# Performance work log

Hardware: AMD Instinct MI355X
Metric: run time of the kernel (lower is better)

Reference implementation:

```python
import jax, jax.numpy as jnp
import numpy as np

# Config constants (match init_kwargs)
E = 16          # n_routed_experts
G = 4           # n_groups
TOPK_G = 2      # topk_groups
K = 4           # n_activated_experts
ROUTE_SCALE = 2.5446


def setup_inputs() -> dict:
    key = jax.random.key(0)
    ks = jax.random.split(key, 9)
    T, D, H = 2048, 1024, 704
    HS = 2 * H  # shared FFN hidden = n_shared_experts * expert_hidden_dim
    sc = lambda k, shape, fan_in: (jax.random.normal(k, shape, jnp.float32)
                                   * (fan_in ** -0.5))
    return {
        "x":      jax.random.normal(ks[0], (T, D), jnp.float32),
        "gate_w": sc(ks[1], (E, D), D),
        "gate_b": jnp.zeros((E,), jnp.float32),       # V3 routing bias (init 0)
        "w1":     sc(ks[2], (E, H, D), D),            # gate proj per expert
        "w3":     sc(ks[3], (E, H, D), D),            # up proj per expert
        "w2":     sc(ks[4], (E, D, H), H),            # down proj per expert
        "ws1":    sc(ks[5], (HS, D), D),              # shared FFN gate proj
        "ws3":    sc(ks[6], (HS, D), D),              # shared FFN up proj
        "ws2":    sc(ks[7], (D, HS), HS),             # shared FFN down proj
    }


def _gate(x, gate_w, gate_b):
    """DeepSeek-V3 sigmoid gate with bias routing + group-limited masking."""
    T = x.shape[0]
    logits = x @ gate_w.T                                   # [T, E]
    scores = jax.nn.sigmoid(logits).astype(jnp.float32)     # original_scores
    routing = scores + gate_b                               # bias only affects routing
    g = routing.reshape(T, G, E // G)
    # use_bias=True -> group score = sum of top-2 routing scores in group
    group_scores = jnp.sum(jax.lax.top_k(g, 2)[0], axis=-1)     # [T, G]
    top_groups = jax.lax.top_k(group_scores, TOPK_G)[1]         # [T, TOPK_G]
    keep = jnp.any(jnp.arange(G)[None, :, None] == top_groups[:, None, :],
                   axis=-1)                                     # [T, G]
    routing = jnp.where(keep[:, :, None], g, -jnp.inf).reshape(T, E)
    idx = jax.lax.top_k(routing, K)[1]                          # [T, K]
    w = jnp.take_along_axis(scores, idx, axis=1)                # un-biased weights
    w = w / jnp.clip(jnp.sum(w, axis=-1, keepdims=True), 1e-9)  # sigmoid renorm
    w = (w * ROUTE_SCALE).astype(x.dtype)
    return w, idx


def reference(x, gate_w, gate_b, w1, w3, w2, ws1, ws3, ws2):
    T, D = x.shape
    weights, idx = _gate(x, gate_w, gate_b)                 # [T,K], [T,K]
    # Dense dispatch/combine matrix: combine[t, e] = gate weight (0 if unrouted)
    combine = jnp.zeros((T, E), x.dtype).at[
        jnp.arange(T)[:, None], idx].add(weights)           # [T, E]
    # Routed experts: SwiGLU per expert, grouped GEMMs
    hg = jnp.einsum('td,ehd->eth', x, w1)                   # [E, T, H]
    hu = jnp.einsum('td,ehd->eth', x, w3)                   # [E, T, H]
    eo = jnp.einsum('eth,edh->etd', jax.nn.silu(hg) * hu, w2)  # [E, T, D]
    y_routed = jnp.einsum('etd,te->td', eo, combine)        # [T, D]
    # Shared experts (always active SwiGLU)
    y_shared = (jax.nn.silu(x @ ws1.T) * (x @ ws3.T)) @ ws2.T
    return y_routed + y_shared
```

## Files before the change

kernel.cpp:

```cpp
#include <hip/hip_runtime.h>
#include <hip/hip_bf16.h>
#include <math.h>

typedef __attribute__((ext_vector_type(4))) float   f32x4;
typedef __attribute__((ext_vector_type(8))) short   short8;
typedef __attribute__((ext_vector_type(8))) __bf16  bf16x8;

union SB8 { short8 s; bf16x8 b; };

__device__ __forceinline__ short f2bf(float f) {
  union { float f; unsigned u; } v; v.f = f;
  unsigned r = v.u + 0x7fffu + ((v.u >> 16) & 1u);
  return (short)(r >> 16);
}

__device__ __forceinline__ short8 cvt8(f32x4 a, f32x4 b) {
  short8 r;
  r[0] = f2bf(a[0]); r[1] = f2bf(a[1]); r[2] = f2bf(a[2]); r[3] = f2bf(a[3]);
  r[4] = f2bf(b[0]); r[5] = f2bf(b[1]); r[6] = f2bf(b[2]); r[7] = f2bf(b[3]);
  return r;
}

__device__ __forceinline__ void ldsload16(const short* g, short* l) {
  __builtin_amdgcn_global_load_lds(
      (const __attribute__((address_space(1))) unsigned int*)g,
      (__attribute__((address_space(3))) unsigned int*)l, 16, 0, 0);
}

#define TT   2048
#define DD   1024
#define HH   704
#define HSS  1408
#define EE   16
#define CAP  2048
#define CSTR 32

#define O1  2097152ULL
#define O2  13631488ULL
#define O3  25165824ULL
#define O4  36700160ULL
#define O5  38141952ULL
#define O6  39583744ULL
#define CVT_TOTAL 41025536ULL

#define W2SZ    11534336ULL
#define WS1SZ   1441792ULL
#define WS1END  26607616ULL
#define CVTA_TOTAL  28049408ULL
#define CVTA_BLOCKS 3424
#define GATE_BLOCKS 512

__global__ __launch_bounds__(256)
void gate_cvt(const float* __restrict__ x,  const float* __restrict__ w1,
              const float* __restrict__ w3, const float* __restrict__ s1,
              const float* __restrict__ s3, short* __restrict__ dst,
              const float* __restrict__ gw, const float* __restrict__ gb,
              int* __restrict__ counts, int* __restrict__ tok,
              float* __restrict__ wgt, int* __restrict__ eslot)
{
  if (blockIdx.x >= GATE_BLOCKS) {
    const int tid = threadIdx.x;
    const size_t base = (size_t)(blockIdx.x - GATE_BLOCKS) * 8192;
    const float* sp[4]; short* dp[4];
    #pragma unroll
    for (int k = 0; k < 4; k++) {
      const size_t sb = base + (size_t)k * 2048;
      const float* src; size_t doff;
      if      (sb < O1)     { src = x  + sb;            doff = sb; }
      else if (sb < O2)     { src = w1 + (sb - O1);     doff = sb; }
      else if (sb < O3)     { src = w3 + (sb - O2);     doff = sb; }
      else if (sb < WS1END) { src = s1 + (sb - O3);     doff = sb + W2SZ; }
      else                  { src = s3 + (sb - WS1END); doff = sb + W2SZ; }
      sp[k] = src + tid * 8;
      dp[k] = dst + doff + tid * 8;
    }
    f32x4 va[8];
    #pragma unroll
    for (int k = 0; k < 4; k++) {
      va[2 * k]     = *(const f32x4*)(sp[k]);
      va[2 * k + 1] = *(const f32x4*)(sp[k] + 4);
    }
    #pragma unroll
    for (int k = 0; k < 4; k++)
      *(short8*)(dp[k]) = cvt8(va[2 * k], va[2 * k + 1]);
    return;
  }

  const int lane = threadIdx.x & 63;
  const int wid  = threadIdx.x >> 6;
  const int t    = blockIdx.x * 4 + wid;
  const int e    = lane & 15;
  const int p    = lane >> 4;

  const float* xp = x + (size_t)t * DD + p * 256;
  const float* gp = gw + (size_t)e * DD + p * 256;

  double a0 = 0.0, a1 = 0.0, a2 = 0.0, a3 = 0.0;
  #pragma unroll 8
  for (int i = 0; i < 64; i++) {
    f32x4 xa = *(const f32x4*)(xp + i * 4);
    f32x4 ga = *(const f32x4*)(gp + i * 4);
    a0 += (double)xa[0] * (double)ga[0];
    a1 += (double)xa[1] * (double)ga[1];
    a2 += (double)xa[2] * (double)ga[2];
    a3 += (double)xa[3] * (double)ga[3];
  }
  double acc = (a0 + a1) + (a2 + a3);
  acc += __shfl_xor(acc, 16);
  acc += __shfl_xor(acc, 32);
  float accf = (float)acc;

  float lf[EE], sc[EE], r[EE];
  #pragma unroll
  for (int j = 0; j < EE; j++) lf[j] = __shfl(accf, j);
  #pragma unroll
  for (int j = 0; j < EE; j++) {
    sc[j] = 1.f / (1.f + expf(-lf[j]));
    r[j] = sc[j] + gb[j];
  }
  float gs[4];
  #pragma unroll
  for (int g = 0; g < 4; g++) {
    float m1 = -1e30f, m2 = -1e30f;
    #pragma unroll
    for (int j = 0; j < 4; j++) {
      float v = r[g * 4 + j];
      if (v > m1) { m2 = m1; m1 = v; }
      else if (v > m2) { m2 = v; }
    }
    gs[g] = m1 + m2;
  }
  int g1 = 0, g2 = -1; float b1 = -1e30f, b2 = -1e30f;
  #pragma unroll
  for (int g = 0; g < 4; g++) {
    if (gs[g] > b1) { b2 = b1; g2 = g1; b1 = gs[g]; g1 = g; }
    else if (gs[g] > b2) { b2 = gs[g]; g2 = g; }
  }
  int idx[4]; float wv[4]; float wsum = 0.f;
  unsigned used = 0;
  #pragma unroll
  for (int k = 0; k < 4; k++) {
    float best = -1e30f; int bi = 0;
    #pragma unroll
    for (int j = 0; j < EE; j++) {
      int g = j >> 2;
      bool keep = (g == g1) || (g == g2);
      if (keep && !((used >> j) & 1) && r[j] > best) { best = r[j]; bi = j; }
    }
    used |= 1u << bi; idx[k] = bi; wv[k] = sc[bi]; wsum += sc[bi];
  }
  float div = wsum < 1e-9f ? 1e-9f : wsum;
  if (lane < 4) {
    float w = wv[lane] / div * 2.5446f;
    int slot = atomicAdd(&counts[idx[lane] * CSTR], 1);
    tok[idx[lane] * CAP + slot] = t;
    wgt[idx[lane] * CAP + slot] = w;
    eslot[t * 4 + lane] = (idx[lane] << 16) | slot;
  }
}

#define WAIT_PREV_TILE()  do { \
    asm volatile("s_waitcnt vmcnt(8)" ::: "memory"); \
    __builtin_amdgcn_sched_barrier(0); \
    __builtin_amdgcn_s_barrier(); \
    __builtin_amdgcn_sched_barrier(0); } while (0)
#define WAIT_LAST_TILE()  do { \
    asm volatile("s_waitcnt vmcnt(0)" ::: "memory"); \
    __builtin_amdgcn_sched_barrier(0); \
    __builtin_amdgcn_s_barrier(); \
    __builtin_amdgcn_sched_barrier(0); } while (0)
#define END_TILE_BARRIER() do { \
    __builtin_amdgcn_sched_barrier(0); \
    __builtin_amdgcn_s_barrier(); } while (0)

__global__ __launch_bounds__(256, 2)
void gemm1_merged(const short* __restrict__ xb, const short* __restrict__ w1b,
                  const short* __restrict__ w3b, const short* __restrict__ ws1b,
                  const short* __restrict__ ws3b, short* __restrict__ act_r,
                  short* __restrict__ act_s, const int* __restrict__ counts,
                  const int* __restrict__ tok,
                  const float* __restrict__ w2f, const float* __restrict__ ws2f,
                  short* __restrict__ w2bd, short* __restrict__ ws2bd)
{
  const int F = blockIdx.x + 11 * (blockIdx.y + 16 * blockIdx.z);
  const int r8 = F & 7, rank = F >> 3;
  int z, Mt, Ntc;
  if (rank < 22) {
    z = 0;
    const int p = rank * 8 + r8;
    Mt = p / 11; Ntc = p - Mt * 11;
  } else if (rank < 374) {
    const int rr = rank - 22;
    z = 1 + r8 + 8 * (rr / 176);
    const int p = rr % 176;
    Mt = p / 11; Ntc = p - Mt * 11;
  } else {
    z = 17;
    const int p = (rank - 374) * 8 + r8;
    Mt = p / 22; Ntc = p - Mt * 22;
  }

  if (z == 0) {
    const int bid = Mt * 11 + Ntc;
    const int tid = threadIdx.x;
    for (int s = 0; s < 9; s++) {
      const size_t base = (size_t)bid * 73728 + (size_t)s * 8192;
      const float* sp[4]; short* dp[4];
      #pragma unroll
      for (int k = 0; k < 4; k++) {
        const size_t sb = base + (size_t)k * 2048;
        if (sb < W2SZ) {
          sp[k] = w2f + sb + tid * 8;
          dp[k] = w2bd + sb + tid * 8;
        } else {
          const size_t o = sb - W2SZ;
          sp[k] = ws2f + o + tid * 8;
          dp[k] = ws2bd + o + tid * 8;
        }
      }
      f32x4 va[8];
      #pragma unroll
      for (int k = 0; k < 4; k++) {
        va[2 * k]     = *(const f32x4*)(sp[k]);
        va[2 * k + 1] = *(const f32x4*)(sp[k] + 4);
      }
      #pragma unroll
      for (int k = 0; k < 4; k++)
        *(short8*)(dp[k]) = cvt8(va[2 * k], va[2 * k + 1]);
    }
    return;
  }

  const bool routed = (z <= EE);
  const int e = z - 1;

  int cnt, N, rowbase = 0;
  const short *W1, *W3;
  short* act;
  if (routed) {
    cnt = counts[e * CSTR];
    if (Mt * 128 >= cnt) return;
    int rb = 0;
    for (int i = 0; i < e; i++) rb += counts[i * CSTR];
    rowbase = rb;
    N = HH;
    W1 = w1b + (size_t)e * HH * DD;
    W3 = w3b + (size_t)e * HH * DD;
    act = act_r;
  } else {
    cnt = TT; N = HSS; W1 = ws1b; W3 = ws3b; act = act_s;
  }
  const int NtB = Ntc * 64;

  __shared__ __align__(16) short lA [2][128 * 64];
  __shared__ __align__(16) short lB1[2][64 * 64];
  __shared__ __align__(16) short lB3[2][64 * 64];

  const int tid = threadIdx.x, lane = tid & 63, wv = tid >> 6;
  const int srow = lane >> 3, schunk = lane & 7, scg = schunk ^ srow;

  const short* pa[4]; const short* pb1[2]; const short* pb3[2];
  #pragma unroll
  for (int i = 0; i < 4; i++) {
    const int g = wv * 4 + i;
    int arow = Mt * 128 + g * 8 + srow;
    if (routed) {
      int slot = arow < cnt ? arow : cnt - 1;
      arow = tok[e * CAP + slot];
    }
    pa[i] = xb + (size_t)arow * DD + scg * 8;
  }
  #pragma unroll
  for (int i = 0; i < 2; i++) {
    const int g = wv * 2 + i;
    const int brow = NtB + g * 8 + srow;
    pb1[i] = W1 + (size_t)brow * DD + scg * 8;
    pb3[i] = W3 + (size_t)brow * DD + scg * 8;
  }

  f32x4 acc1[8], acc3[8];
  #pragma unroll
  for (int i = 0; i < 8; i++) { acc1[i] = (f32x4)0.f; acc3[i] = (f32x4)0.f; }

  const int q = lane >> 4, r7 = lane & 7, hi = (lane & 15) >> 3;

#define STAGE1(c, kk) do { \
    _Pragma("unroll") for (int i = 0; i < 4; i++) \
      ldsload16(pa[i] + (kk),  &lA [c][(wv * 4 + i) * 512]); \
    _Pragma("unroll") for (int i = 0; i < 2; i++) { \
      ldsload16(pb1[i] + (kk), &lB1[c][(wv * 2 + i) * 512]); \
      ldsload16(pb3[i] + (kk), &lB3[c][(wv * 2 + i) * 512]); } } while (0)

#define GEMM1_BODY(c) do { \
    _Pragma("unroll") for (int kc = 0; kc < 2; kc++) { \
      const int cx = (kc * 4 + q) ^ r7; \
      SB8 b1f, b3f; \
      b1f.s = *(const short8*)(&lB1[c][((wv * 2 + hi) * 64 + r7 * 8 + cx) * 8]); \
      b3f.s = *(const short8*)(&lB3[c][((wv * 2 + hi) * 64 + r7 * 8 + cx) * 8]); \
      _Pragma("unroll") for (int mt = 0; mt < 8; mt++) { \
        SB8 af; af.s = *(const short8*)(&lA[c][((2 * mt + hi) * 64 + r7 * 8 + cx) * 8]); \
        acc1[mt] = __builtin_amdgcn_mfma_f32_16x16x32_bf16(af.b, b1f.b, acc1[mt], 0, 0, 0); \
        acc3[mt] = __builtin_amdgcn_mfma_f32_16x16x32_bf16(af.b, b3f.b, acc3[mt], 0, 0, 0); \
      } } } while (0)

  STAGE1(0, 0);
  int cur = 0;
  for (int kk = 64; kk < DD; kk += 64) {
    STAGE1(cur ^ 1, kk);
    WAIT_PREV_TILE();
    GEMM1_BODY(cur);
    END_TILE_BARRIER();
    cur ^= 1;
  }
  WAIT_LAST_TILE();
  GEMM1_BODY(cur);

  const int quad = lane >> 4, lcol = lane & 15;
  const int col = NtB + wv * 16 + lcol;
  #pragma unroll
  for (int mt = 0; mt < 8; mt++) {
    #pragma unroll
    for (int rg = 0; rg < 4; rg++) {
      const int r = Mt * 128 + mt * 16 + quad * 4 + rg;
      if (r < cnt) {
        float g = acc1[mt][rg], u = acc3[mt][rg];
        float a = g / (1.f + __expf(-g)) * u;
        act[(size_t)(rowbase + r) * N + col] = f2bf(a);
      }
    }
  }
#undef STAGE1
#undef GEMM1_BODY
}

__global__ __launch_bounds__(256, 2)
void gemm2_merged(const short* __restrict__ act_r, const short* __restrict__ act_s,
                  const short* __restrict__ w2b, const short* __restrict__ ws2b,
                  float* __restrict__ y, float* __restrict__ outr,
                  const int* __restrict__ counts, const float* __restrict__ wgt)
{
  const int F = blockIdx.x + 8 * (blockIdx.y + 16 * blockIdx.z);
  const int r8 = F & 7, rank = F >> 3;
  int z, Mt, Nt;
  if (rank < 256) {
    z = r8 + 8 * (rank >> 7);
    const int p = rank & 127;
    Mt = p >> 3; Nt = p & 7;
  } else {
    z = 16;
    const int p = (rank - 256) * 8 + r8;
    Mt = p >> 3; Nt = p & 7;
  }

  const bool routed = (z < EE);

  int cnt, Kd, rowbase = 0;
  const short *A, *W;
  if (routed) {
    cnt = counts[z * CSTR];
    if (Mt * 128 >= cnt) return;
    int rb = 0;
    for (int i = 0; i < z; i++) rb += counts[i * CSTR];
    rowbase = rb;
    Kd = HH;
    A = act_r + (size_t)rowbase * HH;
    W = w2b + (size_t)z * DD * HH;
  } else {
    cnt = TT; Kd = HSS; A = act_s; W = ws2b;
  }

  __shared__ __align__(16) short lA[2][128 * 64];
  __shared__ __align__(16) short lB[2][128 * 64];

  const int tid = threadIdx.x, lane = tid & 63, wv = tid >> 6;
  const int srow = lane >> 3, schunk = lane & 7, scg = schunk ^ srow;

  const short* pa[4]; const short* pb[4];
  #pragma unroll
  for (int i = 0; i < 4; i++) {
    const int g = wv * 4 + i;
    int arow = Mt * 128 + g * 8 + srow;
    if (arow >= cnt) arow = cnt - 1;
    pa[i] = A + (size_t)arow * Kd + scg * 8;
    const int brow = Nt * 128 + g * 8 + srow;
    pb[i] = W + (size_t)brow * Kd + scg * 8;
  }

  f32x4 acc[8][2];
  #pragma unroll
  for (int i = 0; i < 8; i++) { acc[i][0] = (f32x4)0.f; acc[i][1] = (f32x4)0.f; }

  const int q = lane >> 4, r7 = lane & 7, hi = (lane & 15) >> 3;

#define STAGE2(c, kk) do { \
    _Pragma("unroll") for (int i = 0; i < 4; i++) { \
      const int g = wv * 4 + i; \
      ldsload16(pa[i] + (kk), &lA[c][g * 512]); \
      ldsload16(pb[i] + (kk), &lB[c][g * 512]); } } while (0)

#define GEMM2_BODY(c) do { \
    _Pragma("unroll") for (int kc = 0; kc < 2; kc++) { \
      const int cx = (kc * 4 + q) ^ r7; \
      SB8 bf[2]; \
      _Pragma("unroll") for (int ntl = 0; ntl < 2; ntl++) { \
        const int a16 = ((wv * 2 + ntl) * 2 + hi) * 64 + r7 * 8 + cx; \
        bf[ntl].s = *(const short8*)(&lB[c][a16 * 8]); \
      } \
      _Pragma("unroll") for (int mt = 0; mt < 8; mt++) { \
        const int a16 = (2 * mt + hi) * 64 + r7 * 8 + cx; \
        SB8 af; af.s = *(const short8*)(&lA[c][a16 * 8]); \
        acc[mt][0] = __builtin_amdgcn_mfma_f32_16x16x32_bf16(af.b, bf[0].b, acc[mt][0], 0, 0, 0); \
        acc[mt][1] = __builtin_amdgcn_mfma_f32_16x16x32_bf16(af.b, bf[1].b, acc[mt][1], 0, 0, 0); \
      } } } while (0)

  STAGE2(0, 0);
  int cur = 0;
  for (int kk = 64; kk < Kd; kk += 64) {
    STAGE2(cur ^ 1, kk);
    WAIT_PREV_TILE();
    GEMM2_BODY(cur);
    END_TILE_BARRIER();
    cur ^= 1;
  }
  WAIT_LAST_TILE();
  GEMM2_BODY(cur);

  const int quad = lane >> 4, lcol = lane & 15;
  #pragma unroll
  for (int mt = 0; mt < 8; mt++) {
    #pragma unroll
    for (int ntl = 0; ntl < 2; ntl++) {
      const int col = Nt * 128 + (wv * 2 + ntl) * 16 + lcol;
      #pragma unroll
      for (int rg = 0; rg < 4; rg++) {
        const int slot = Mt * 128 + mt * 16 + quad * 4 + rg;
        const float v = acc[mt][ntl][rg];
        if (routed) {
          if (slot < cnt) {
            const float w = wgt[z * CAP + slot];
            outr[(size_t)(rowbase + slot) * DD + col] = w * v;
          }
        } else {
          y[(size_t)slot * DD + col] = v;
        }
      }
    }
  }
#undef STAGE2
#undef GEMM2_BODY
}

__global__ __launch_bounds__(256)
void combine_kernel(float* __restrict__ y, const float* __restrict__ outr,
                    const int* __restrict__ eslot, const int* __restrict__ counts)
{
  const int t = blockIdx.x;
  const int d = threadIdx.x * 4;

  int offs[EE];
  int s = 0;
  #pragma unroll
  for (int i = 0; i < EE; i++) { offs[i] = s; s += counts[i * CSTR]; }

  f32x4 accv = *(f32x4*)(y + (size_t)t * DD + d);
  #pragma unroll
  for (int k = 0; k < 4; k++) {
    const int es = eslot[t * 4 + k];
    const int row = offs[es >> 16] + (es & 0xFFFF);
    accv += *(const f32x4*)(outr + (size_t)row * DD + d);
  }
  *(f32x4*)(y + (size_t)t * DD + d) = accv;
}

extern "C" void kernel_launch(void* const* d_in, const int* in_sizes, int n_in,
                              void* d_out, int out_size, void* d_ws, size_t ws_size,
                              hipStream_t stream) {
  const float* x      = (const float*)d_in[0];
  const float* gate_w = (const float*)d_in[1];
  const float* gate_b = (const float*)d_in[2];
  const float* w1     = (const float*)d_in[3];
  const float* w3     = (const float*)d_in[4];
  const float* w2     = (const float*)d_in[5];
  const float* ws1    = (const float*)d_in[6];
  const float* ws3    = (const float*)d_in[7];
  const float* ws2    = (const float*)d_in[8];
  float* y = (float*)d_out;

  char* ws = (char*)d_ws;
  int*   counts = (int*)ws;
  int*   tok    = (int*)(ws + 2048);
  float* wgt    = (float*)(ws + 2048 + (size_t)EE * CAP * 4);
  int*   eslot  = (int*)(ws + 2048 + (size_t)EE * CAP * 8);
  short* bf     = (short*)(ws + 2048 + (size_t)EE * CAP * 8 + (size_t)TT * 16);
  short* xb   = bf;
  short* w1b  = bf + O1;
  short* w3b  = bf + O2;
  short* w2b  = bf + O3;
  short* ws1b = bf + O4;
  short* ws3b = bf + O5;
  short* ws2b = bf + O6;
  short* act_r = bf + CVT_TOTAL;
  short* act_s = act_r + (size_t)8192 * HH;
  float* outr = (float*)(bf + O1);

  (void)hipMemsetAsync(counts, 0, EE * CSTR * sizeof(int), stream);

  gate_cvt<<<GATE_BLOCKS + CVTA_BLOCKS, 256, 0, stream>>>(
      x, w1, w3, ws1, ws3, bf,
      gate_w, gate_b, counts, tok, wgt, eslot);

  gemm1_merged<<<dim3(11, TT / 128, EE + 3), 256, 0, stream>>>(
      xb, w1b, w3b, ws1b, ws3b, act_r, act_s, counts, tok,
      w2, ws2, w2b, ws2b);

  gemm2_merged<<<dim3(DD / 128, TT / 128, EE + 1), 256, 0, stream>>>(
      act_r, act_s, w2b, ws2b, y, outr, counts, wgt);

  combine_kernel<<<TT, 256, 0, stream>>>(y, outr, eslot, counts);
}
```

Baseline: 316.5 us.

## Double block size to 512 threads, splitting M tile across two wave groups

```diff
diff --git a/kernel.cpp b/kernel.cpp
--- a/kernel.cpp
+++ b/kernel.cpp
@@ -160,7 +160,7 @@
 }
 
 #define WAIT_PREV_TILE()  do { \
-    asm volatile("s_waitcnt vmcnt(8)" ::: "memory"); \
+    asm volatile("s_waitcnt vmcnt(4)" ::: "memory"); \
     __builtin_amdgcn_sched_barrier(0); \
     __builtin_amdgcn_s_barrier(); \
     __builtin_amdgcn_sched_barrier(0); } while (0)
@@ -173,7 +173,7 @@
     __builtin_amdgcn_sched_barrier(0); \
     __builtin_amdgcn_s_barrier(); } while (0)
 
-__global__ __launch_bounds__(256, 2)
+__global__ __launch_bounds__(512, 2)
 void gemm1_merged(const short* __restrict__ xb, const short* __restrict__ w1b,
                   const short* __restrict__ w3b, const short* __restrict__ ws1b,
                   const short* __restrict__ ws3b, short* __restrict__ act_r,
@@ -203,12 +203,12 @@
   if (z == 0) {
     const int bid = Mt * 11 + Ntc;
     const int tid = threadIdx.x;
-    for (int s = 0; s < 9; s++) {
-      const size_t base = (size_t)bid * 73728 + (size_t)s * 8192;
-      const float* sp[4]; short* dp[4];
+    for (int s = 0; s < 3; s++) {
+      const size_t base = (size_t)bid * 73728 + (size_t)s * 24576;
+      const float* sp[6]; short* dp[6];
       #pragma unroll
-      for (int k = 0; k < 4; k++) {
-        const size_t sb = base + (size_t)k * 2048;
+      for (int k = 0; k < 6; k++) {
+        const size_t sb = base + (size_t)k * 4096;
         if (sb < W2SZ) {
           sp[k] = w2f + sb + tid * 8;
           dp[k] = w2bd + sb + tid * 8;
@@ -218,14 +218,14 @@
           dp[k] = ws2bd + o + tid * 8;
         }
       }
-      f32x4 va[8];
+      f32x4 va[12];
       #pragma unroll
-      for (int k = 0; k < 4; k++) {
+      for (int k = 0; k < 6; k++) {
         va[2 * k]     = *(const f32x4*)(sp[k]);
         va[2 * k + 1] = *(const f32x4*)(sp[k] + 4);
       }
       #pragma unroll
-      for (int k = 0; k < 4; k++)
+      for (int k = 0; k < 6; k++)
         *(short8*)(dp[k]) = cvt8(va[2 * k], va[2 * k + 1]);
     }
     return;
@@ -259,10 +259,10 @@
   const int tid = threadIdx.x, lane = tid & 63, wv = tid >> 6;
   const int srow = lane >> 3, schunk = lane & 7, scg = schunk ^ srow;
 
-  const short* pa[4]; const short* pb1[2]; const short* pb3[2];
-  #pragma unroll
-  for (int i = 0; i < 4; i++) {
-    const int g = wv * 4 + i;
+  const short* pa[2]; const short* pb1; const short* pb3;
+  #pragma unroll
+  for (int i = 0; i < 2; i++) {
+    const int g = wv * 2 + i;
     int arow = Mt * 128 + g * 8 + srow;
     if (routed) {
       int slot = arow < cnt ? arow : cnt - 1;
@@ -270,35 +270,33 @@
     }
     pa[i] = xb + (size_t)arow * DD + scg * 8;
   }
-  #pragma unroll
-  for (int i = 0; i < 2; i++) {
-    const int g = wv * 2 + i;
-    const int brow = NtB + g * 8 + srow;
-    pb1[i] = W1 + (size_t)brow * DD + scg * 8;
-    pb3[i] = W3 + (size_t)brow * DD + scg * 8;
-  }
-
-  f32x4 acc1[8], acc3[8];
-  #pragma unroll
-  for (int i = 0; i < 8; i++) { acc1[i] = (f32x4)0.f; acc3[i] = (f32x4)0.f; }
+  {
+    const int brow = NtB + wv * 8 + srow;
+    pb1 = W1 + (size_t)brow * DD + scg * 8;
+    pb3 = W3 + (size_t)brow * DD + scg * 8;
+  }
+
+  f32x4 acc1[4], acc3[4];
+  #pragma unroll
+  for (int i = 0; i < 4; i++) { acc1[i] = (f32x4)0.f; acc3[i] = (f32x4)0.f; }
 
   const int q = lane >> 4, r7 = lane & 7, hi = (lane & 15) >> 3;
+  const int wc = wv & 3, mh = wv >> 2;
 
 #define STAGE1(c, kk) do { \
-    _Pragma("unroll") for (int i = 0; i < 4; i++) \
-      ldsload16(pa[i] + (kk),  &lA [c][(wv * 4 + i) * 512]); \
-    _Pragma("unroll") for (int i = 0; i < 2; i++) { \
-      ldsload16(pb1[i] + (kk), &lB1[c][(wv * 2 + i) * 512]); \
-      ldsload16(pb3[i] + (kk), &lB3[c][(wv * 2 + i) * 512]); } } while (0)
+    ldsload16(pa[0] + (kk), &lA [c][(wv * 2 + 0) * 512]); \
+    ldsload16(pa[1] + (kk), &lA [c][(wv * 2 + 1) * 512]); \
+    ldsload16(pb1  + (kk),  &lB1[c][wv * 512]); \
+    ldsload16(pb3  + (kk),  &lB3[c][wv * 512]); } while (0)
 
 #define GEMM1_BODY(c) do { \
     _Pragma("unroll") for (int kc = 0; kc < 2; kc++) { \
       const int cx = (kc * 4 + q) ^ r7; \
       SB8 b1f, b3f; \
-      b1f.s = *(const short8*)(&lB1[c][((wv * 2 + hi) * 64 + r7 * 8 + cx) * 8]); \
-      b3f.s = *(const short8*)(&lB3[c][((wv * 2 + hi) * 64 + r7 * 8 + cx) * 8]); \
-      _Pragma("unroll") for (int mt = 0; mt < 8; mt++) { \
-        SB8 af; af.s = *(const short8*)(&lA[c][((2 * mt + hi) * 64 + r7 * 8 + cx) * 8]); \
+      b1f.s = *(const short8*)(&lB1[c][((wc * 2 + hi) * 64 + r7 * 8 + cx) * 8]); \
+      b3f.s = *(const short8*)(&lB3[c][((wc * 2 + hi) * 64 + r7 * 8 + cx) * 8]); \
+      _Pragma("unroll") for (int mt = 0; mt < 4; mt++) { \
+        SB8 af; af.s = *(const short8*)(&lA[c][((2 * (mh * 4 + mt) + hi) * 64 + r7 * 8 + cx) * 8]); \
         acc1[mt] = __builtin_amdgcn_mfma_f32_16x16x32_bf16(af.b, b1f.b, acc1[mt], 0, 0, 0); \
         acc3[mt] = __builtin_amdgcn_mfma_f32_16x16x32_bf16(af.b, b3f.b, acc3[mt], 0, 0, 0); \
       } } } while (0)
@@ -316,12 +314,12 @@
   GEMM1_BODY(cur);
 
   const int quad = lane >> 4, lcol = lane & 15;
-  const int col = NtB + wv * 16 + lcol;
-  #pragma unroll
-  for (int mt = 0; mt < 8; mt++) {
+  const int col = NtB + wc * 16 + lcol;
+  #pragma unroll
+  for (int mt = 0; mt < 4; mt++) {
     #pragma unroll
     for (int rg = 0; rg < 4; rg++) {
-      const int r = Mt * 128 + mt * 16 + quad * 4 + rg;
+      const int r = Mt * 128 + (mh * 4 + mt) * 16 + quad * 4 + rg;
       if (r < cnt) {
         float g = acc1[mt][rg], u = acc3[mt][rg];
         float a = g / (1.f + __expf(-g)) * u;
@@ -333,7 +331,7 @@
 #undef GEMM1_BODY
 }
 
-__global__ __launch_bounds__(256, 2)
+__global__ __launch_bounds__(512, 2)
 void gemm2_merged(const short* __restrict__ act_r, const short* __restrict__ act_s,
                   const short* __restrict__ w2b, const short* __restrict__ ws2b,
                   float* __restrict__ y, float* __restrict__ outr,
@@ -375,10 +373,10 @@
   const int tid = threadIdx.x, lane = tid & 63, wv = tid >> 6;
   const int srow = lane >> 3, schunk = lane & 7, scg = schunk ^ srow;
 
-  const short* pa[4]; const short* pb[4];
-  #pragma unroll
-  for (int i = 0; i < 4; i++) {
-    const int g = wv * 4 + i;
+  const short* pa[2]; const short* pb[2];
+  #pragma unroll
+  for (int i = 0; i < 2; i++) {
+    const int g = wv * 2 + i;
     int arow = Mt * 128 + g * 8 + srow;
     if (arow >= cnt) arow = cnt - 1;
     pa[i] = A + (size_t)arow * Kd + scg * 8;
@@ -386,28 +384,29 @@
     pb[i] = W + (size_t)brow * Kd + scg * 8;
   }
 
-  f32x4 acc[8][2];
-  #pragma unroll
-  for (int i = 0; i < 8; i++) { acc[i][0] = (f32x4)0.f; acc[i][1] = (f32x4)0.f; }
+  f32x4 acc[4][2];
+  #pragma unroll
+  for (int i = 0; i < 4; i++) { acc[i][0] = (f32x4)0.f; acc[i][1] = (f32x4)0.f; }
 
   const int q = lane >> 4, r7 = lane & 7, hi = (lane & 15) >> 3;
+  const int wc = wv & 3, mh = wv >> 2;
 
 #define STAGE2(c, kk) do { \
-    _Pragma("unroll") for (int i = 0; i < 4; i++) { \
-      const int g = wv * 4 + i; \
-      ldsload16(pa[i] + (kk), &lA[c][g * 512]); \
-      ldsload16(pb[i] + (kk), &lB[c][g * 512]); } } while (0)
+    ldsload16(pa[0] + (kk), &lA[c][(wv * 2 + 0) * 512]); \
+    ldsload16(pa[1] + (kk), &lA[c][(wv * 2 + 1) * 512]); \
+    ldsload16(pb[0] + (kk), &lB[c][(wv * 2 + 0) * 512]); \
+    ldsload16(pb[1] + (kk), &lB[c][(wv * 2 + 1) * 512]); } while (0)
 
 #define GEMM2_BODY(c) do { \
     _Pragma("unroll") for (int kc = 0; kc < 2; kc++) { \
       const int cx = (kc * 4 + q) ^ r7; \
       SB8 bf[2]; \
       _Pragma("unroll") for (int ntl = 0; ntl < 2; ntl++) { \
-        const int a16 = ((wv * 2 + ntl) * 2 + hi) * 64 + r7 * 8 + cx; \
+        const int a16 = ((wc * 2 + ntl) * 2 + hi) * 64 + r7 * 8 + cx; \
         bf[ntl].s = *(const short8*)(&lB[c][a16 * 8]); \
       } \
-      _Pragma("unroll") for (int mt = 0; mt < 8; mt++) { \
-        const int a16 = (2 * mt + hi) * 64 + r7 * 8 + cx; \
+      _Pragma("unroll") for (int mt = 0; mt < 4; mt++) { \
+        const int a16 = (2 * (mh * 4 + mt) + hi) * 64 + r7 * 8 + cx; \
         SB8 af; af.s = *(const short8*)(&lA[c][a16 * 8]); \
         acc[mt][0] = __builtin_amdgcn_mfma_f32_16x16x32_bf16(af.b, bf[0].b, acc[mt][0], 0, 0, 0); \
         acc[mt][1] = __builtin_amdgcn_mfma_f32_16x16x32_bf16(af.b, bf[1].b, acc[mt][1], 0, 0, 0); \
@@ -427,13 +426,13 @@
 
   const int quad = lane >> 4, lcol = lane & 15;
   #pragma unroll
-  for (int mt = 0; mt < 8; mt++) {
+  for (int mt = 0; mt < 4; mt++) {
     #pragma unroll
     for (int ntl = 0; ntl < 2; ntl++) {
-      const int col = Nt * 128 + (wv * 2 + ntl) * 16 + lcol;
+      const int col = Nt * 128 + (wc * 2 + ntl) * 16 + lcol;
       #pragma unroll
       for (int rg = 0; rg < 4; rg++) {
-        const int slot = Mt * 128 + mt * 16 + quad * 4 + rg;
+        const int slot = Mt * 128 + (mh * 4 + mt) * 16 + quad * 4 + rg;
         const float v = acc[mt][ntl][rg];
         if (routed) {
           if (slot < cnt) {
@@ -509,11 +508,11 @@
       x, w1, w3, ws1, ws3, bf,
       gate_w, gate_b, counts, tok, wgt, eslot);
 
-  gemm1_merged<<<dim3(11, TT / 128, EE + 3), 256, 0, stream>>>(
+  gemm1_merged<<<dim3(11, TT / 128, EE + 3), 512, 0, stream>>>(
       xb, w1b, w3b, ws1b, ws3b, act_r, act_s, counts, tok,
       w2, ws2, w2b, ws2b);
 
-  gemm2_merged<<<dim3(DD / 128, TT / 128, EE + 1), 256, 0, stream>>>(
+  gemm2_merged<<<dim3(DD / 128, TT / 128, EE + 1), 512, 0, stream>>>(
       act_r, act_s, w2b, ws2b, y, outr, counts, wgt);
 
   combine_kernel<<<TT, 256, 0, stream>>>(y, outr, eslot, counts);
```

Measured after the change: 300.6 us. -5.0%, faster.
